# Kernel optimization log

Hardware: AMD Instinct MI355X
Metric: run time of the kernel (lower is better)

The kernel has to match this reference:

```python
import jax
import jax.numpy as jnp
import numpy as np
from jax import lax

TOKENS = 65536
D = 512
E = 8
H = 2048


def setup_inputs() -> dict:
    key = jax.random.key(0)
    ks = jax.random.split(key, 6)
    inp = {
        "x": jax.random.normal(ks[0], (TOKENS, D), dtype=jnp.float32),
        "router_w": jax.random.normal(ks[1], (D, E), dtype=jnp.float32) * 0.02,
        "router_b": jnp.zeros((E,), dtype=jnp.float32),
        "w1": jax.random.normal(ks[2], (E, D, H), dtype=jnp.float32) * 0.02,
        "b1": jnp.zeros((E, H), dtype=jnp.float32),
        "w2": jax.random.normal(ks[3], (E, H, D), dtype=jnp.float32) * 0.02,
        "b2": jnp.zeros((E, D), dtype=jnp.float32),
        "act_expert_num": 2,
    }
    return inp


def reference(x, router_w, router_b, w1, b1, w2, b2, act_expert_num):
    B = x.shape[0]
    # Router: Linear + Softmax over experts
    probs = jax.nn.softmax(x @ router_w + router_b, axis=-1)  # [B, E]
    rw, sel = lax.top_k(probs, act_expert_num)                # [B, k]
    rw = rw / jnp.sum(rw, axis=-1, keepdims=True)             # renormalize top-k
    # Dense combine weights per expert: comb[b, e] = sum_k rw[b,k] * [sel[b,k]==e]
    comb = jnp.zeros((B, E), dtype=x.dtype).at[
        jnp.arange(B)[:, None], sel
    ].add(rw)                                                 # [B, E]

    def body(acc, params):
        w1e, b1e, w2e, b2e, ce = params
        h = jax.nn.relu(x @ w1e + b1e)        # [B, H]
        y = h @ w2e + b2e                     # [B, D]
        return acc + ce[:, None] * y, None

    out, _ = lax.scan(body, jnp.zeros_like(x), (w1, b1, w2, b2, comb.T))
    return out
```

## Files before the change

### kernel.cpp

```cpp
#include <hip/hip_runtime.h>
#include <hip/hip_bf16.h>

constexpr int B = 65536;
constexpr int D = 512;
constexpr int E = 8;
constexpr int H = 2048;
constexpr int CT_ST = 140;

typedef __bf16 bf16x8 __attribute__((ext_vector_type(8)));
typedef float  f32x4  __attribute__((ext_vector_type(4)));

__device__ __forceinline__ unsigned short f2bf(float f) {
    unsigned u = __float_as_uint(f);
    u += 0x7FFFu + ((u >> 16) & 1u);
    return (unsigned short)(u >> 16);
}

__device__ __forceinline__ void dma16(const void* g, void* lds) {
    auto* gp = reinterpret_cast<const __attribute__((address_space(1))) unsigned*>(
        reinterpret_cast<uintptr_t>(g));
    auto* lp = reinterpret_cast<__attribute__((address_space(3))) unsigned*>(
        reinterpret_cast<uintptr_t>(lds));
    __builtin_amdgcn_global_load_lds(gp, lp, 16, 0, 0);
}

__global__ __launch_bounds__(256) void convert_x(
    const float* __restrict__ x, unsigned short* __restrict__ xb) {
    const size_t i = ((size_t)blockIdx.x * 256 + threadIdx.x) * 8;
    const float4 v0 = *(const float4*)(x + i);
    const float4 v1 = *(const float4*)(x + i + 4);
    uint4 p;
    p.x = (unsigned)f2bf(v0.x) | ((unsigned)f2bf(v0.y) << 16);
    p.y = (unsigned)f2bf(v0.z) | ((unsigned)f2bf(v0.w) << 16);
    p.z = (unsigned)f2bf(v1.x) | ((unsigned)f2bf(v1.y) << 16);
    p.w = (unsigned)f2bf(v1.z) | ((unsigned)f2bf(v1.w) << 16);
    *(uint4*)(xb + i) = p;
}

__global__ __launch_bounds__(128) void router2(
    const float* __restrict__ x, const float* __restrict__ rw,
    const float* __restrict__ rb, unsigned* __restrict__ cnt,
    unsigned* __restrict__ tok_list, float* __restrict__ w_list) {
    __shared__ unsigned lcnt[E];
    __shared__ unsigned gbase[E];
    const int tid = threadIdx.x;
    if (tid < E) lcnt[tid] = 0u;
    __syncthreads();

    const int t = blockIdx.x * 128 + tid;
    const float4* xr = (const float4*)(x + (size_t)t * D);
    float acc[E];
#pragma unroll
    for (int e = 0; e < E; ++e) acc[e] = 0.f;

    for (int i = 0; i < D / 4; ++i) {
        const float4 xv = xr[i];
        const float* wr = rw + (size_t)i * 4 * E;
#pragma unroll
        for (int e = 0; e < E; ++e) {
            acc[e] += xv.x * wr[e] + xv.y * wr[E + e] + xv.z * wr[2 * E + e]
                    + xv.w * wr[3 * E + e];
        }
    }
#pragma unroll
    for (int e = 0; e < E; ++e) acc[e] += rb[e];

    int e0 = 0; float l0 = acc[0];
#pragma unroll
    for (int e = 1; e < E; ++e) if (acc[e] > l0) { l0 = acc[e]; e0 = e; }
    int e1 = -1; float l1 = -3.4e38f;
#pragma unroll
    for (int e = 0; e < E; ++e)
        if (e != e0 && acc[e] > l1) { l1 = acc[e]; e1 = e; }

    const float w0 = 1.f / (1.f + expf(l1 - l0));
    const float w1v = 1.f - w0;

    const unsigned r0 = atomicAdd(&lcnt[e0], 1u);
    const unsigned r1 = atomicAdd(&lcnt[e1], 1u);
    __syncthreads();
    if (tid < E) gbase[tid] = atomicAdd(&cnt[tid], lcnt[tid]);
    __syncthreads();
    const unsigned s0 = gbase[e0] + r0;
    const unsigned s1 = gbase[e1] + r1;
    tok_list[(size_t)e0 * B + s0] = (unsigned)t;  w_list[(size_t)e0 * B + s0] = w0;
    tok_list[(size_t)e1 * B + s1] = (unsigned)t;  w_list[(size_t)e1 * B + s1] = w1v;
}

__global__ __launch_bounds__(128) void pad_counts(
    const unsigned* __restrict__ cnt, unsigned* __restrict__ cntp,
    unsigned* __restrict__ tok_list, float* __restrict__ w_list, int cap) {
    const int tid = threadIdx.x;
    for (int e = 0; e < E; ++e) {
        const unsigned c = cnt[e];
        unsigned p = (c + 127u) & ~127u;
        if (p > (unsigned)cap) p = (unsigned)cap;
        if (c + tid < p) {
            tok_list[(size_t)e * B + c + tid] = 0u;
            w_list[(size_t)e * B + c + tid] = 0.f;
        }
        if (tid == 0) cntp[e] = p;
    }
}

__global__ __launch_bounds__(256) void pack_bf16(
    const float* __restrict__ in, unsigned short* __restrict__ outp,
    int R, int C) {
    __shared__ unsigned short T[64][72];
    const int e = blockIdx.z;
    const int c0 = blockIdx.x * 64, r0 = blockIdx.y * 64;
    const float* ine = in + (size_t)e * R * C;
    unsigned short* oute = outp + (size_t)e * R * C;
    const int tid = threadIdx.x;
    const int rl = tid >> 2, cl = (tid & 3) * 16;

    const float* src = ine + (size_t)(r0 + rl) * C + c0 + cl;
    unsigned pk[8];
#pragma unroll
    for (int i = 0; i < 4; ++i) {
        const float4 v = *(const float4*)(src + i * 4);
        pk[2 * i]     = (unsigned)f2bf(v.x) | ((unsigned)f2bf(v.y) << 16);
        pk[2 * i + 1] = (unsigned)f2bf(v.z) | ((unsigned)f2bf(v.w) << 16);
    }
    *(uint4*)(&T[rl][cl])     = make_uint4(pk[0], pk[1], pk[2], pk[3]);
    *(uint4*)(&T[rl][cl + 8]) = make_uint4(pk[4], pk[5], pk[6], pk[7]);
    __syncthreads();

    unsigned po[8];
#pragma unroll
    for (int j = 0; j < 8; ++j) {
        po[j] = (unsigned)T[cl + 2 * j][rl] | ((unsigned)T[cl + 2 * j + 1][rl] << 16);
    }
    unsigned short* dst = oute + ((size_t)((r0 + cl) >> 5) * C + (c0 + rl)) * 32
                               + ((r0 + cl) & 31);
    *(uint4*)(dst)     = make_uint4(po[0], po[1], po[2], po[3]);
    *(uint4*)(dst + 8) = make_uint4(po[4], po[5], po[6], po[7]);
}

struct alignas(16) StageBufs {
    unsigned short A[2][128 * 32];
    unsigned short Bm[2][128 * 32];
};
union SmemU {
    StageBufs st;
    unsigned short Ct[64 * CT_ST];
};

__global__ __launch_bounds__(256, 4) void stage_kernel(
    const unsigned short* __restrict__ xb,
    const unsigned short* __restrict__ w1p, const unsigned short* __restrict__ w2p,
    const float* __restrict__ b1, const float* __restrict__ b2,
    const unsigned* __restrict__ cntp,
    const unsigned* __restrict__ tok_list, const float* __restrict__ w_list,
    unsigned short* __restrict__ hb_w, const unsigned short* __restrict__ hb_r,
    float* __restrict__ out, int e_w, int e_r, int cap) {
    __shared__ SmemU sm;
    const int tid = threadIdx.x, wv = tid >> 6, lane = tid & 63;
    const int ln = lane & 15, q = lane >> 4;
    const int wm = wv & 1, wn = wv >> 1;
    const int r4 = lane >> 2, pc = lane & 3;
    const int dst0 = (wv * 2 + 0) * 512;
    const int dst1 = (wv * 2 + 1) * 512;
    const int qs  = q  ^ ((ln >> 1) & 3);
    const int pcs = pc ^ ((r4 >> 1) & 3);

    const int NX = gridDim.x;
    const int l  = blockIdx.y * NX + blockIdx.x;
    const bool is_g2 = (l < 4 * NX);

    f32x4 acc[4][4];
#pragma unroll
    for (int i = 0; i < 4; ++i)
#pragma unroll
        for (int j = 0; j < 4; ++j) acc[i][j] = (f32x4){0.f, 0.f, 0.f, 0.f};

    if (!is_g2) {
        if (e_w < 0) return;
        const int e = e_w;
        const int l2 = l - 4 * NX;
        const int chunk = l2 >> 7, w = l2 & 127;
        const int xg = (chunk << 3) + (w & 7), yn = w >> 3;
        const int m0 = xg * 128;
        if ((unsigned)m0 >= cntp[e]) return;
        const int n0 = yn * 128;
        const size_t base = (size_t)e * B;
        constexpr int NT = D / 32;

        const unsigned ta0 = tok_list[base + m0 + (wv * 2 + 0) * 16 + r4];
        const unsigned ta1 = tok_list[base + m0 + (wv * 2 + 1) * 16 + r4];
        const unsigned short* ap0 = xb + (size_t)ta0 * D + pcs * 8;
        const unsigned short* ap1 = xb + (size_t)ta1 * D + pcs * 8;
        const unsigned short* w1e = w1p + (size_t)e * H * D;
        const unsigned short* bp0 = w1e + (size_t)(n0 + (wv * 2 + 0) * 16 + r4) * 32 + pcs * 8;
        const unsigned short* bp1 = w1e + (size_t)(n0 + (wv * 2 + 1) * 16 + r4) * 32 + pcs * 8;
        const size_t bstep = (size_t)H * 32;

        unsigned short *A0 = sm.st.A[0], *A1 = sm.st.A[1];
        unsigned short *B0 = sm.st.Bm[0], *B1 = sm.st.Bm[1];

        dma16(ap0, A0 + dst0);  dma16(ap1, A0 + dst1);
        dma16(bp0, B0 + dst0);  dma16(bp1, B0 + dst1);

        for (int t = 0; t < NT; ++t) {
            asm volatile("s_waitcnt vmcnt(0)" ::: "memory");
            __builtin_amdgcn_s_barrier();
            asm volatile("" ::: "memory");
            if (t + 1 < NT) {
                const int ka = (t + 1) * 32;
                const size_t kb = (size_t)(t + 1) * bstep;
                dma16(ap0 + ka, A1 + dst0);  dma16(ap1 + ka, A1 + dst1);
                dma16(bp0 + kb, B1 + dst0);  dma16(bp1 + kb, B1 + dst1);
            }
            bf16x8 af[4], bfr[4];
#pragma unroll
            for (int i = 0; i < 4; ++i) {
                af[i]  = *(const bf16x8*)(A0 + (wm * 64 + i * 16 + ln) * 32 + qs * 8);
                bfr[i] = *(const bf16x8*)(B0 + (wn * 64 + i * 16 + ln) * 32 + qs * 8);
            }
            __builtin_amdgcn_s_setprio(1);
#pragma unroll
            for (int mt = 0; mt < 4; ++mt)
#pragma unroll
                for (int nt = 0; nt < 4; ++nt)
                    acc[mt][nt] = __builtin_amdgcn_mfma_f32_16x16x32_bf16(
                        af[mt], bfr[nt], acc[mt][nt], 0, 0, 0);
            __builtin_amdgcn_s_setprio(0);
            unsigned short* tp;
            tp = A0; A0 = A1; A1 = tp;
            tp = B0; B0 = B1; B1 = tp;
        }
        __syncthreads();

        float b1v[4];
#pragma unroll
        for (int nt = 0; nt < 4; ++nt)
            b1v[nt] = b1[(size_t)e * H + n0 + wn * 64 + nt * 16 + ln];

#pragma unroll
        for (int c = 0; c < 2; ++c) {
            if (wm == c) {
#pragma unroll
                for (int mt = 0; mt < 4; ++mt)
#pragma unroll
                    for (int nt = 0; nt < 4; ++nt)
#pragma unroll
                        for (int r = 0; r < 4; ++r) {
                            const int lr = mt * 16 + q * 4 + r;
                            float v = acc[mt][nt][r] + b1v[nt];
                            v = v > 0.f ? v : 0.f;
                            sm.Ct[lr * CT_ST + wn * 64 + nt * 16 + ln] = f2bf(v);
                        }
            }
            __syncthreads();
            {
                const int cc = wv;
#pragma unroll
                for (int u = 0; u < 4; ++u) {
                    const int sr = u * 16 + (lane >> 2);
                    const unsigned short* csrc = sm.Ct + sr * CT_ST + cc * 32 + (lane & 3) * 8;
                    unsigned short* gdst = hb_w
                        + ((size_t)((n0 >> 5) + cc) * cap + (m0 + c * 64 + sr)) * 32
                        + (lane & 3) * 8;
                    *(uint4*)gdst = *(const uint4*)csrc;
                }
            }
            __syncthreads();
        }
    } else {
        if (e_r < 0) return;
        const int e = e_r;
        const int chunk = l >> 5, w = l & 31;
        const int xg = (chunk << 3) + (w & 7), yn = w >> 3;
        const int m0 = xg * 128;
        if ((unsigned)m0 >= cntp[e]) return;
        const int n0 = yn * 128;
        const size_t base = (size_t)e * B;
        constexpr int NT = H / 32;

        const unsigned short* ap0 = hb_r + (size_t)(m0 + (wv * 2 + 0) * 16 + r4) * 32 + pcs * 8;
        const unsigned short* ap1 = hb_r + (size_t)(m0 + (wv * 2 + 1) * 16 + r4) * 32 + pcs * 8;
        const unsigned short* w2e = w2p + (size_t)e * D * H;
        const unsigned short* bp0 = w2e + (size_t)(n0 + (wv * 2 + 0) * 16 + r4) * 32 + pcs * 8;
        const unsigned short* bp1 = w2e + (size_t)(n0 + (wv * 2 + 1) * 16 + r4) * 32 + pcs * 8;
        const size_t astep = (size_t)cap * 32;
        const size_t bstep = (size_t)D * 32;

        unsigned short *A0 = sm.st.A[0], *A1 = sm.st.A[1];
        unsigned short *B0 = sm.st.Bm[0], *B1 = sm.st.Bm[1];

        dma16(ap0, A0 + dst0);  dma16(ap1, A0 + dst1);
        dma16(bp0, B0 + dst0);  dma16(bp1, B0 + dst1);

        for (int t = 0; t < NT; ++t) {
            asm volatile("s_waitcnt vmcnt(0)" ::: "memory");
            __builtin_amdgcn_s_barrier();
            asm volatile("" ::: "memory");
            if (t + 1 < NT) {
                const size_t ka = (size_t)(t + 1) * astep;
                const size_t kb = (size_t)(t + 1) * bstep;
                dma16(ap0 + ka, A1 + dst0);  dma16(ap1 + ka, A1 + dst1);
                dma16(bp0 + kb, B1 + dst0);  dma16(bp1 + kb, B1 + dst1);
            }
            bf16x8 af[4], bfr[4];
#pragma unroll
            for (int i = 0; i < 4; ++i) {
                af[i]  = *(const bf16x8*)(A0 + (wm * 64 + i * 16 + ln) * 32 + qs * 8);
                bfr[i] = *(const bf16x8*)(B0 + (wn * 64 + i * 16 + ln) * 32 + qs * 8);
            }
            __builtin_amdgcn_s_setprio(1);
#pragma unroll
            for (int mt = 0; mt < 4; ++mt)
#pragma unroll
                for (int nt = 0; nt < 4; ++nt)
                    acc[mt][nt] = __builtin_amdgcn_mfma_f32_16x16x32_bf16(
                        af[mt], bfr[nt], acc[mt][nt], 0, 0, 0);
            __builtin_amdgcn_s_setprio(0);
            unsigned short* tp;
            tp = A0; A0 = A1; A1 = tp;
            tp = B0; B0 = B1; B1 = tp;
        }
        __syncthreads();

        float b2v[4];
#pragma unroll
        for (int nt = 0; nt < 4; ++nt)
            b2v[nt] = b2[(size_t)e * D + n0 + wn * 64 + nt * 16 + ln];

#pragma unroll
        for (int mt = 0; mt < 4; ++mt) {
#pragma unroll
            for (int r = 0; r < 4; ++r) {
                const int m = wm * 64 + mt * 16 + q * 4 + r;
                const float wgt = w_list[base + m0 + m];
                if (wgt != 0.f) {
                    const int tok = (int)tok_list[base + m0 + m];
                    float* orow = out + (size_t)tok * D + n0 + wn * 64 + ln;
#pragma unroll
                    for (int nt = 0; nt < 4; ++nt)
                        orow[nt * 16] += wgt * (acc[mt][nt][r] + b2v[nt]);
                }
            }
        }
    }
}

extern "C" void kernel_launch(void* const* d_in, const int* in_sizes, int n_in,
                              void* d_out, int out_size, void* d_ws, size_t ws_size,
                              hipStream_t stream) {
    const float* x  = (const float*)d_in[0];
    const float* rw = (const float*)d_in[1];
    const float* rb = (const float*)d_in[2];
    const float* w1 = (const float*)d_in[3];
    const float* b1 = (const float*)d_in[4];
    const float* w2 = (const float*)d_in[5];
    const float* b2 = (const float*)d_in[6];
    float* out = (float*)d_out;

    char* ws = (char*)d_ws;
    const size_t off_tok = 1024;
    const size_t off_wl  = off_tok + (size_t)E * B * 4;
    const size_t off_w1s = off_wl  + (size_t)E * B * 4;
    const size_t off_w2s = off_w1s + (size_t)E * D * H * 2;
    const size_t off_xb  = off_w2s + (size_t)E * D * H * 2;
    const size_t off_hb  = off_xb  + (size_t)B * D * 2;

    unsigned* cnt      = (unsigned*)ws;
    unsigned* cntp     = (unsigned*)(ws + 256);
    unsigned* tok_list = (unsigned*)(ws + off_tok);
    float*    w_list   = (float*)(ws + off_wl);
    unsigned short* w1s = (unsigned short*)(ws + off_w1s);
    unsigned short* w2s = (unsigned short*)(ws + off_w2s);
    unsigned short* xb  = (unsigned short*)(ws + off_xb);

    const size_t rem = (ws_size > off_hb) ? (ws_size - off_hb) : 0;
    const size_t hrow = (size_t)H * 2;
    int cap; bool pipelined;
    {
        size_t cp = (rem / 2 / hrow) & ~(size_t)1023;
        if (cp > 24576) cp = 24576;
        if (cp >= 20480) { pipelined = true; cap = (int)cp; }
        else {
            pipelined = false;
            size_t cs = (rem / hrow) & ~(size_t)1023;
            if (cs > 24576) cs = 24576;
            cap = (int)cs;
        }
    }
    unsigned short* hb0 = (unsigned short*)(ws + off_hb);
    unsigned short* hb1 = pipelined ? hb0 + (size_t)cap * H : hb0;

    hipMemsetAsync(ws, 0, 1024, stream);
    hipMemsetAsync(d_out, 0, (size_t)out_size * sizeof(float), stream);

    convert_x<<<(B * D) / 2048, 256, 0, stream>>>(x, xb);
    pack_bf16<<<dim3(H / 64, D / 64, E), 256, 0, stream>>>(w1, w1s, D, H);
    pack_bf16<<<dim3(D / 64, H / 64, E), 256, 0, stream>>>(w2, w2s, H, D);
    router2<<<B / 128, 128, 0, stream>>>(x, rw, rb, cnt, tok_list, w_list);
    pad_counts<<<1, 128, 0, stream>>>(cnt, cntp, tok_list, w_list, cap);

    const dim3 sgrid(cap / 128, 20);
    if (pipelined) {
        for (int s = 0; s <= E; ++s) {
            unsigned short* hw = (s & 1) ? hb1 : hb0;
            unsigned short* hr = (s & 1) ? hb0 : hb1;
            stage_kernel<<<sgrid, 256, 0, stream>>>(
                xb, w1s, w2s, b1, b2, cntp, tok_list, w_list,
                hw, hr, out, (s < E) ? s : -1, (s > 0) ? s - 1 : -1, cap);
        }
    } else {
        for (int e = 0; e < E; ++e) {
            stage_kernel<<<sgrid, 256, 0, stream>>>(
                xb, w1s, w2s, b1, b2, cntp, tok_list, w_list,
                hb0, hb0, out, e, -1, cap);
            stage_kernel<<<sgrid, 256, 0, stream>>>(
                xb, w1s, w2s, b1, b2, cntp, tok_list, w_list,
                hb0, hb0, out, -1, e, cap);
        }
    }
}
```

Baseline: 1.168 ms.

## Enlarge expert GEMM tiles to 256 rows with 8 waves and triple-buffered prefetch

```diff
diff --git a/kernel.cpp b/kernel.cpp
--- a/kernel.cpp
+++ b/kernel.cpp
@@ -87,13 +87,13 @@
     tok_list[(size_t)e1 * B + s1] = (unsigned)t;  w_list[(size_t)e1 * B + s1] = w1v;
 }
 
-__global__ __launch_bounds__(128) void pad_counts(
+__global__ __launch_bounds__(256) void pad_counts(
     const unsigned* __restrict__ cnt, unsigned* __restrict__ cntp,
     unsigned* __restrict__ tok_list, float* __restrict__ w_list, int cap) {
     const int tid = threadIdx.x;
     for (int e = 0; e < E; ++e) {
         const unsigned c = cnt[e];
-        unsigned p = (c + 127u) & ~127u;
+        unsigned p = (c + 255u) & ~255u;
         if (p > (unsigned)cap) p = (unsigned)cap;
         if (c + tid < p) {
             tok_list[(size_t)e * B + c + tid] = 0u;
@@ -138,15 +138,15 @@
 }
 
 struct alignas(16) StageBufs {
-    unsigned short A[2][128 * 32];
-    unsigned short Bm[2][128 * 32];
+    unsigned short A[3][256 * 32];
+    unsigned short Bm[3][128 * 32];
 };
 union SmemU {
     StageBufs st;
     unsigned short Ct[64 * CT_ST];
 };
 
-__global__ __launch_bounds__(256, 4) void stage_kernel(
+__global__ __launch_bounds__(512, 4) void stage_kernel(
     const unsigned short* __restrict__ xb,
     const unsigned short* __restrict__ w1p, const unsigned short* __restrict__ w2p,
     const float* __restrict__ b1, const float* __restrict__ b2,
@@ -157,10 +157,11 @@
     __shared__ SmemU sm;
     const int tid = threadIdx.x, wv = tid >> 6, lane = tid & 63;
     const int ln = lane & 15, q = lane >> 4;
-    const int wm = wv & 1, wn = wv >> 1;
+    const int wm = wv & 3, wn = wv >> 2;
     const int r4 = lane >> 2, pc = lane & 3;
-    const int dst0 = (wv * 2 + 0) * 512;
-    const int dst1 = (wv * 2 + 1) * 512;
+    const int dstA0 = (wv * 2 + 0) * 512;
+    const int dstA1 = (wv * 2 + 1) * 512;
+    const int dstB  = wv * 512;
     const int qs  = q  ^ ((ln >> 1) & 3);
     const int pcs = pc ^ ((r4 >> 1) & 3);
 
@@ -180,7 +181,7 @@
         const int l2 = l - 4 * NX;
         const int chunk = l2 >> 7, w = l2 & 127;
         const int xg = (chunk << 3) + (w & 7), yn = w >> 3;
-        const int m0 = xg * 128;
+        const int m0 = xg * 256;
         if ((unsigned)m0 >= cntp[e]) return;
         const int n0 = yn * 128;
         const size_t base = (size_t)e * B;
@@ -191,25 +192,26 @@
         const unsigned short* ap0 = xb + (size_t)ta0 * D + pcs * 8;
         const unsigned short* ap1 = xb + (size_t)ta1 * D + pcs * 8;
         const unsigned short* w1e = w1p + (size_t)e * H * D;
-        const unsigned short* bp0 = w1e + (size_t)(n0 + (wv * 2 + 0) * 16 + r4) * 32 + pcs * 8;
-        const unsigned short* bp1 = w1e + (size_t)(n0 + (wv * 2 + 1) * 16 + r4) * 32 + pcs * 8;
+        const unsigned short* bp0 = w1e + (size_t)(n0 + wv * 16 + r4) * 32 + pcs * 8;
         const size_t bstep = (size_t)H * 32;
 
-        unsigned short *A0 = sm.st.A[0], *A1 = sm.st.A[1];
-        unsigned short *B0 = sm.st.Bm[0], *B1 = sm.st.Bm[1];
-
-        dma16(ap0, A0 + dst0);  dma16(ap1, A0 + dst1);
-        dma16(bp0, B0 + dst0);  dma16(bp1, B0 + dst1);
+        unsigned short *A0 = sm.st.A[0], *A1 = sm.st.A[1], *A2 = sm.st.A[2];
+        unsigned short *B0 = sm.st.Bm[0], *B1 = sm.st.Bm[1], *B2 = sm.st.Bm[2];
+
+        dma16(ap0, A0 + dstA0);  dma16(ap1, A0 + dstA1);  dma16(bp0, B0 + dstB);
+        dma16(ap0 + 32, A1 + dstA0);  dma16(ap1 + 32, A1 + dstA1);
+        dma16(bp0 + bstep, B1 + dstB);
 
         for (int t = 0; t < NT; ++t) {
-            asm volatile("s_waitcnt vmcnt(0)" ::: "memory");
+            if (t + 1 < NT) { asm volatile("s_waitcnt vmcnt(3)" ::: "memory"); }
+            else            { asm volatile("s_waitcnt vmcnt(0)" ::: "memory"); }
             __builtin_amdgcn_s_barrier();
             asm volatile("" ::: "memory");
-            if (t + 1 < NT) {
-                const int ka = (t + 1) * 32;
-                const size_t kb = (size_t)(t + 1) * bstep;
-                dma16(ap0 + ka, A1 + dst0);  dma16(ap1 + ka, A1 + dst1);
-                dma16(bp0 + kb, B1 + dst0);  dma16(bp1 + kb, B1 + dst1);
+            if (t + 2 < NT) {
+                const int ka = (t + 2) * 32;
+                const size_t kb = (size_t)(t + 2) * bstep;
+                dma16(ap0 + ka, A2 + dstA0);  dma16(ap1 + ka, A2 + dstA1);
+                dma16(bp0 + kb, B2 + dstB);
             }
             bf16x8 af[4], bfr[4];
 #pragma unroll
@@ -226,8 +228,8 @@
                         af[mt], bfr[nt], acc[mt][nt], 0, 0, 0);
             __builtin_amdgcn_s_setprio(0);
             unsigned short* tp;
-            tp = A0; A0 = A1; A1 = tp;
-            tp = B0; B0 = B1; B1 = tp;
+            tp = A0; A0 = A1; A1 = A2; A2 = tp;
+            tp = B0; B0 = B1; B1 = B2; B2 = tp;
         }
         __syncthreads();
 
@@ -237,7 +239,7 @@
             b1v[nt] = b1[(size_t)e * H + n0 + wn * 64 + nt * 16 + ln];
 
 #pragma unroll
-        for (int c = 0; c < 2; ++c) {
+        for (int c = 0; c < 4; ++c) {
             if (wm == c) {
 #pragma unroll
                 for (int mt = 0; mt < 4; ++mt)
@@ -253,14 +255,14 @@
             }
             __syncthreads();
             {
-                const int cc = wv;
-#pragma unroll
-                for (int u = 0; u < 4; ++u) {
-                    const int sr = u * 16 + (lane >> 2);
-                    const unsigned short* csrc = sm.Ct + sr * CT_ST + cc * 32 + (lane & 3) * 8;
+#pragma unroll
+                for (int u = 0; u < 2; ++u) {
+                    const int fl = tid * 2 + u;
+                    const int sr = fl >> 4, slot = fl & 15;
+                    const unsigned short* csrc = sm.Ct + sr * CT_ST + slot * 8;
                     unsigned short* gdst = hb_w
-                        + ((size_t)((n0 >> 5) + cc) * cap + (m0 + c * 64 + sr)) * 32
-                        + (lane & 3) * 8;
+                        + ((size_t)((n0 >> 5) + (slot >> 2)) * cap + (m0 + c * 64 + sr)) * 32
+                        + (slot & 3) * 8;
                     *(uint4*)gdst = *(const uint4*)csrc;
                 }
             }
@@ -271,7 +273,7 @@
         const int e = e_r;
         const int chunk = l >> 5, w = l & 31;
         const int xg = (chunk << 3) + (w & 7), yn = w >> 3;
-        const int m0 = xg * 128;
+        const int m0 = xg * 256;
         if ((unsigned)m0 >= cntp[e]) return;
         const int n0 = yn * 128;
         const size_t base = (size_t)e * B;
@@ -280,26 +282,27 @@
         const unsigned short* ap0 = hb_r + (size_t)(m0 + (wv * 2 + 0) * 16 + r4) * 32 + pcs * 8;
         const unsigned short* ap1 = hb_r + (size_t)(m0 + (wv * 2 + 1) * 16 + r4) * 32 + pcs * 8;
         const unsigned short* w2e = w2p + (size_t)e * D * H;
-        const unsigned short* bp0 = w2e + (size_t)(n0 + (wv * 2 + 0) * 16 + r4) * 32 + pcs * 8;
-        const unsigned short* bp1 = w2e + (size_t)(n0 + (wv * 2 + 1) * 16 + r4) * 32 + pcs * 8;
+        const unsigned short* bp0 = w2e + (size_t)(n0 + wv * 16 + r4) * 32 + pcs * 8;
         const size_t astep = (size_t)cap * 32;
         const size_t bstep = (size_t)D * 32;
 
-        unsigned short *A0 = sm.st.A[0], *A1 = sm.st.A[1];
-        unsigned short *B0 = sm.st.Bm[0], *B1 = sm.st.Bm[1];
-
-        dma16(ap0, A0 + dst0);  dma16(ap1, A0 + dst1);
-        dma16(bp0, B0 + dst0);  dma16(bp1, B0 + dst1);
+        unsigned short *A0 = sm.st.A[0], *A1 = sm.st.A[1], *A2 = sm.st.A[2];
+        unsigned short *B0 = sm.st.Bm[0], *B1 = sm.st.Bm[1], *B2 = sm.st.Bm[2];
+
+        dma16(ap0, A0 + dstA0);  dma16(ap1, A0 + dstA1);  dma16(bp0, B0 + dstB);
+        dma16(ap0 + astep, A1 + dstA0);  dma16(ap1 + astep, A1 + dstA1);
+        dma16(bp0 + bstep, B1 + dstB);
 
         for (int t = 0; t < NT; ++t) {
-            asm volatile("s_waitcnt vmcnt(0)" ::: "memory");
+            if (t + 1 < NT) { asm volatile("s_waitcnt vmcnt(3)" ::: "memory"); }
+            else            { asm volatile("s_waitcnt vmcnt(0)" ::: "memory"); }
             __builtin_amdgcn_s_barrier();
             asm volatile("" ::: "memory");
-            if (t + 1 < NT) {
-                const size_t ka = (size_t)(t + 1) * astep;
-                const size_t kb = (size_t)(t + 1) * bstep;
-                dma16(ap0 + ka, A1 + dst0);  dma16(ap1 + ka, A1 + dst1);
-                dma16(bp0 + kb, B1 + dst0);  dma16(bp1 + kb, B1 + dst1);
+            if (t + 2 < NT) {
+                const size_t ka = (size_t)(t + 2) * astep;
+                const size_t kb = (size_t)(t + 2) * bstep;
+                dma16(ap0 + ka, A2 + dstA0);  dma16(ap1 + ka, A2 + dstA1);
+                dma16(bp0 + kb, B2 + dstB);
             }
             bf16x8 af[4], bfr[4];
 #pragma unroll
@@ -316,8 +319,8 @@
                         af[mt], bfr[nt], acc[mt][nt], 0, 0, 0);
             __builtin_amdgcn_s_setprio(0);
             unsigned short* tp;
-            tp = A0; A0 = A1; A1 = tp;
-            tp = B0; B0 = B1; B1 = tp;
+            tp = A0; A0 = A1; A1 = A2; A2 = tp;
+            tp = B0; B0 = B1; B1 = B2; B2 = tp;
         }
         __syncthreads();
 
@@ -376,12 +379,12 @@
     const size_t hrow = (size_t)H * 2;
     int cap; bool pipelined;
     {
-        size_t cp = (rem / 2 / hrow) & ~(size_t)1023;
+        size_t cp = (rem / 2 / hrow) & ~(size_t)2047;
         if (cp > 24576) cp = 24576;
         if (cp >= 20480) { pipelined = true; cap = (int)cp; }
         else {
             pipelined = false;
-            size_t cs = (rem / hrow) & ~(size_t)1023;
+            size_t cs = (rem / hrow) & ~(size_t)2047;
             if (cs > 24576) cs = 24576;
             cap = (int)cs;
         }
@@ -396,23 +399,23 @@
     pack_bf16<<<dim3(H / 64, D / 64, E), 256, 0, stream>>>(w1, w1s, D, H);
     pack_bf16<<<dim3(D / 64, H / 64, E), 256, 0, stream>>>(w2, w2s, H, D);
     router2<<<B / 128, 128, 0, stream>>>(x, rw, rb, cnt, tok_list, w_list);
-    pad_counts<<<1, 128, 0, stream>>>(cnt, cntp, tok_list, w_list, cap);
-
-    const dim3 sgrid(cap / 128, 20);
+    pad_counts<<<1, 256, 0, stream>>>(cnt, cntp, tok_list, w_list, cap);
+
+    const dim3 sgrid(cap / 256, 20);
     if (pipelined) {
         for (int s = 0; s <= E; ++s) {
             unsigned short* hw = (s & 1) ? hb1 : hb0;
             unsigned short* hr = (s & 1) ? hb0 : hb1;
-            stage_kernel<<<sgrid, 256, 0, stream>>>(
+            stage_kernel<<<sgrid, 512, 0, stream>>>(
                 xb, w1s, w2s, b1, b2, cntp, tok_list, w_list,
                 hw, hr, out, (s < E) ? s : -1, (s > 0) ? s - 1 : -1, cap);
         }
     } else {
         for (int e = 0; e < E; ++e) {
-            stage_kernel<<<sgrid, 256, 0, stream>>>(
+            stage_kernel<<<sgrid, 512, 0, stream>>>(
                 xb, w1s, w2s, b1, b2, cntp, tok_list, w_list,
                 hb0, hb0, out, e, -1, cap);
-            stage_kernel<<<sgrid, 256, 0, stream>>>(
+            stage_kernel<<<sgrid, 512, 0, stream>>>(
                 xb, w1s, w2s, b1, b2, cntp, tok_list, w_list,
                 hb0, hb0, out, -1, e, cap);
         }
```

New measurement: 1.187 ms. About the same (+1.7%).
